# Kernel tuning notes

Hardware: AMD Instinct MI355X
Metric: run time of the kernel (lower is better)

The kernel has to match this reference:

```python
import jax, jax.numpy as jnp
import numpy as np

PATCH = 9  # patch_size (kernel_size=1, stride=1, padding=0, dilation_patch=1)


def setup_inputs() -> dict:
    key = jax.random.key(0)
    k1, k2 = jax.random.split(key)
    B, C, H, W = 4, 256, 128, 128
    return {
        "input1": jax.random.normal(k1, (B, C, H, W), dtype=jnp.float32),
        "input2": jax.random.normal(k2, (B, C, H, W), dtype=jnp.float32),
    }


def _correlation(input1, input2, patch=PATCH):
    # Faithful to torch _correlation_patch_based fast path:
    # corr[b, dy*P+dx, h, w] = sum_c input1[b,c,h,w] * input2_pad[b,c,h+dy,w+dx]
    # where input2 is zero-padded by P//2 (matches F.unfold padding=P//2).
    B, C, H, W = input1.shape
    pad = patch // 2
    i2p = jnp.pad(input2, ((0, 0), (0, 0), (pad, pad), (pad, pad)))
    # displacement offsets in unfold order: ky-major, kx-minor
    offs = jnp.stack(
        jnp.meshgrid(jnp.arange(patch), jnp.arange(patch), indexing="ij"), axis=-1
    ).reshape(-1, 2)  # (P*P, 2)

    def body(carry, off):
        # shifted window of input2, same (B,C,H,W) footprint (no unfold blowup)
        win = jax.lax.dynamic_slice(i2p, (0, 0, off[0], off[1]), (B, C, H, W))
        return carry, jnp.einsum("bchw,bchw->bhw", input1, win)

    _, corr = jax.lax.scan(body, None, offs)  # (P*P, B, H, W)
    return jnp.transpose(corr, (1, 0, 2, 3))  # (B, P*P, H, W)


def reference(input1, input2):
    return _correlation(input1, input2)
```

## Files before the change

### kernel.cpp

```cpp
#include <hip/hip_runtime.h>

#define BB   4
#define CC   256
#define HH   128
#define WW   128
#define PAD  4
#define KOUT 81

#define TH   8
#define SW   16
#define KC   32
#define NCHUNK (CC / KC)
#define AK   40

typedef _Float16 half8 __attribute__((ext_vector_type(8)));
typedef float    f32x4 __attribute__((ext_vector_type(4)));

__global__ __launch_bounds__(512, 4)
void corr_mfma4(const float* __restrict__ i1,
                const float* __restrict__ i2,
                float* __restrict__ out)
{
    __shared__ _Float16 Ald[128 * AK];
    __shared__ _Float16 Bld[512 * AK];

    const int t    = threadIdx.x;
    const int wave = t >> 6;
    const int lane = t & 63;
    const int l15  = lane & 15;
    const int quad = lane >> 4;

    const int raw     = blockIdx.x + 8 * blockIdx.y + 128 * blockIdx.z;
    const int logical = (raw & 7) * 64 + (raw >> 3);
    const int b  = logical >> 7;
    const int h0 = ((logical >> 3) & 15) * TH;
    const int w0 = (logical & 7) * SW;

    const size_t strideC = (size_t)HH * WW;
    const float* i1b = i1 + (size_t)b * CC * strideC;
    const float* i2b = i2 + (size_t)b * CC * strideC;

    bool valid;
    const float* gp;
    _Float16* ld0;

    if (t < 384) {
        const int g   = t % 6;
        const int t6  = t / 6;
        const int ch8 = t6 & 3;
        const int sr  = t6 >> 2;
        const int row  = h0 - PAD + sr;
        const int col0 = w0 - PAD + 4 * g;
        valid = (row >= 0) && (row < HH) && (col0 >= 0) && (col0 + 3 < WW);
        gp  = i2b + (size_t)(valid ? row : 0) * WW + (valid ? col0 : 0)
                  + (size_t)ch8 * 8 * strideC;
        ld0 = &Bld[(sr * 32 + 4 * g) * AK + ch8 * 8];
    } else {
        const int i   = t - 384;
        const int g   = i & 3;
        const int t4  = i >> 2;
        const int ch8 = t4 & 3;
        const int sr  = t4 >> 2;
        valid = true;
        gp  = i1b + (size_t)(h0 + sr) * WW + (w0 + 4 * g)
                  + (size_t)ch8 * 8 * strideC;
        ld0 = &Ald[(sr * 16 + 4 * g) * AK + ch8 * 8];
    }

    f32x4 acc[9][2];
#pragma unroll
    for (int dy = 0; dy < 9; ++dy) {
        acc[dy][0] = (f32x4){0.f, 0.f, 0.f, 0.f};
        acc[dy][1] = (f32x4){0.f, 0.f, 0.f, 0.f};
    }

    f32x4 L[8];

    if (valid) {
#pragma unroll
        for (int j = 0; j < 8; ++j)
            L[j] = *(const f32x4*)(gp + (size_t)j * strideC);
#pragma unroll
        for (int i = 0; i < 4; ++i) {
            half8 hv;
#pragma unroll
            for (int k = 0; k < 8; ++k) hv[k] = (_Float16)L[k][i];
            *(half8*)(ld0 + i * AK) = hv;
        }
    } else {
        const half8 z = (half8){0, 0, 0, 0, 0, 0, 0, 0};
#pragma unroll
        for (int i = 0; i < 4; ++i)
            *(half8*)(ld0 + i * AK) = z;
    }
    __syncthreads();

#pragma unroll 1
    for (int ch = 0; ch < NCHUNK; ++ch) {
        if (valid && (ch + 1 < NCHUNK)) {
            const float* gnext = gp + (size_t)(ch + 1) * KC * strideC;
#pragma unroll
            for (int j = 0; j < 8; ++j)
                L[j] = *(const f32x4*)(gnext + (size_t)j * strideC);
        }

        {
            const half8 a = *(const half8*)&Ald[(wave * 16 + l15) * AK + quad * 8];
#pragma unroll
            for (int dy = 0; dy < 9; ++dy) {
                const int r = wave + dy;
                const half8 b0 = *(const half8*)&Bld[(r * 32 + l15) * AK + quad * 8];
                acc[dy][0] = __builtin_amdgcn_mfma_f32_16x16x32_f16(a, b0, acc[dy][0], 0, 0, 0);
                const half8 b1 = *(const half8*)&Bld[(r * 32 + 16 + l15) * AK + quad * 8];
                acc[dy][1] = __builtin_amdgcn_mfma_f32_16x16x32_f16(a, b1, acc[dy][1], 0, 0, 0);
            }
        }

        if (ch + 1 < NCHUNK) {
            __syncthreads();
            if (valid) {
#pragma unroll
                for (int i = 0; i < 4; ++i) {
                    half8 hv;
#pragma unroll
                    for (int k = 0; k < 8; ++k) hv[k] = (_Float16)L[k][i];
                    *(half8*)(ld0 + i * AK) = hv;
                }
            }
            __syncthreads();
        }
    }

    const int h = h0 + wave;
#pragma unroll
    for (int dy = 0; dy < 9; ++dy) {
#pragma unroll
        for (int tt = 0; tt < 2; ++tt) {
#pragma unroll
            for (int reg = 0; reg < 4; ++reg) {
                const int p  = quad * 4 + reg;
                const int dx = l15 + 16 * tt - p;
                if (dx >= 0 && dx <= 8) {
                    out[(((size_t)b * KOUT + (dy * 9 + dx)) * HH + h) * WW + (w0 + p)] =
                        acc[dy][tt][reg];
                }
            }
        }
    }
}

extern "C" void kernel_launch(void* const* d_in, const int* in_sizes, int n_in,
                              void* d_out, int out_size, void* d_ws, size_t ws_size,
                              hipStream_t stream)
{
    (void)in_sizes; (void)n_in; (void)d_ws; (void)ws_size; (void)out_size;
    const float* i1 = (const float*)d_in[0];
    const float* i2 = (const float*)d_in[1];
    float* out = (float*)d_out;

    dim3 grid(WW / SW, HH / TH, BB);
    dim3 block(512);
    corr_mfma4<<<grid, block, 0, stream>>>(i1, i2, out);
}
```

Measured before the change: 178.1 us.

## Stage output through shared memory and interleave fp16 conversion between MFMA groups

```diff
diff --git a/kernel.cpp b/kernel.cpp
--- a/kernel.cpp
+++ b/kernel.cpp
@@ -12,17 +12,20 @@
 #define KC   32
 #define NCHUNK (CC / KC)
 #define AK   40
+#define SCP  130
 
 typedef _Float16 half8 __attribute__((ext_vector_type(8)));
 typedef float    f32x4 __attribute__((ext_vector_type(4)));
 
 __global__ __launch_bounds__(512, 4)
-void corr_mfma4(const float* __restrict__ i1,
+void corr_mfma5(const float* __restrict__ i1,
                 const float* __restrict__ i2,
                 float* __restrict__ out)
 {
-    __shared__ _Float16 Ald[128 * AK];
-    __shared__ _Float16 Bld[512 * AK];
+    __shared__ __align__(16) char smem[51200];
+    _Float16* const Ald = (_Float16*)smem;
+    _Float16* const Bld = (_Float16*)(smem + 10240);
+    float*    const sc  = (float*)smem;
 
     const int t    = threadIdx.x;
     const int wave = t >> 6;
@@ -74,18 +77,17 @@
         acc[dy][1] = (f32x4){0.f, 0.f, 0.f, 0.f};
     }
 
-    f32x4 L[8];
-
     if (valid) {
+        f32x4 L[8];
 #pragma unroll
         for (int j = 0; j < 8; ++j)
             L[j] = *(const f32x4*)(gp + (size_t)j * strideC);
 #pragma unroll
         for (int i = 0; i < 4; ++i) {
-            half8 hv;
+            half8 hvp;
 #pragma unroll
-            for (int k = 0; k < 8; ++k) hv[k] = (_Float16)L[k][i];
-            *(half8*)(ld0 + i * AK) = hv;
+            for (int k = 0; k < 8; ++k) hvp[k] = (_Float16)L[k][i];
+            *(half8*)(ld0 + i * AK) = hvp;
         }
     } else {
         const half8 z = (half8){0, 0, 0, 0, 0, 0, 0, 0};
@@ -95,43 +97,65 @@
     }
     __syncthreads();
 
+    half8 hv[4];
+
 #pragma unroll 1
     for (int ch = 0; ch < NCHUNK; ++ch) {
-        if (valid && (ch + 1 < NCHUNK)) {
-            const float* gnext = gp + (size_t)(ch + 1) * KC * strideC;
+        const bool more = (ch + 1 < NCHUNK);
+
+        f32x4 L[8];
+        if (valid && more) {
+            const float* g = gp + (size_t)(ch + 1) * KC * strideC;
 #pragma unroll
             for (int j = 0; j < 8; ++j)
-                L[j] = *(const f32x4*)(gnext + (size_t)j * strideC);
+                L[j] = *(const f32x4*)(g + (size_t)j * strideC);
         }
 
-        {
-            const half8 a = *(const half8*)&Ald[(wave * 16 + l15) * AK + quad * 8];
+        const half8 a = *(const half8*)&Ald[(wave * 16 + l15) * AK + quad * 8];
+
 #pragma unroll
-            for (int dy = 0; dy < 9; ++dy) {
-                const int r = wave + dy;
-                const half8 b0 = *(const half8*)&Bld[(r * 32 + l15) * AK + quad * 8];
-                acc[dy][0] = __builtin_amdgcn_mfma_f32_16x16x32_f16(a, b0, acc[dy][0], 0, 0, 0);
-                const half8 b1 = *(const half8*)&Bld[(r * 32 + 16 + l15) * AK + quad * 8];
-                acc[dy][1] = __builtin_amdgcn_mfma_f32_16x16x32_f16(a, b1, acc[dy][1], 0, 0, 0);
+        for (int dy = 0; dy < 5; ++dy) {
+            const int r = wave + dy;
+            const half8 b0 = *(const half8*)&Bld[(r * 32 + l15) * AK + quad * 8];
+            acc[dy][0] = __builtin_amdgcn_mfma_f32_16x16x32_f16(a, b0, acc[dy][0], 0, 0, 0);
+            const half8 b1 = *(const half8*)&Bld[(r * 32 + 16 + l15) * AK + quad * 8];
+            acc[dy][1] = __builtin_amdgcn_mfma_f32_16x16x32_f16(a, b1, acc[dy][1], 0, 0, 0);
+        }
+
+        if (valid && more) {
+#pragma unroll
+            for (int i = 0; i < 4; ++i) {
+#pragma unroll
+                for (int k = 0; k < 4; ++k) hv[i][k] = (_Float16)L[k][i];
+            }
+#pragma unroll
+            for (int i = 0; i < 4; ++i) {
+#pragma unroll
+                for (int k = 4; k < 8; ++k) hv[i][k] = (_Float16)L[k][i];
             }
         }
 
-        if (ch + 1 < NCHUNK) {
+#pragma unroll
+        for (int dy = 5; dy < 9; ++dy) {
+            const int r = wave + dy;
+            const half8 b0 = *(const half8*)&Bld[(r * 32 + l15) * AK + quad * 8];
+            acc[dy][0] = __builtin_amdgcn_mfma_f32_16x16x32_f16(a, b0, acc[dy][0], 0, 0, 0);
+            const half8 b1 = *(const half8*)&Bld[(r * 32 + 16 + l15) * AK + quad * 8];
+            acc[dy][1] = __builtin_amdgcn_mfma_f32_16x16x32_f16(a, b1, acc[dy][1], 0, 0, 0);
+        }
+
+        if (more) {
             __syncthreads();
             if (valid) {
 #pragma unroll
-                for (int i = 0; i < 4; ++i) {
-                    half8 hv;
-#pragma unroll
-                    for (int k = 0; k < 8; ++k) hv[k] = (_Float16)L[k][i];
-                    *(half8*)(ld0 + i * AK) = hv;
-                }
+                for (int i = 0; i < 4; ++i)
+                    *(half8*)(ld0 + i * AK) = hv[i];
             }
             __syncthreads();
         }
     }
 
-    const int h = h0 + wave;
+    __syncthreads();
 #pragma unroll
     for (int dy = 0; dy < 9; ++dy) {
 #pragma unroll
@@ -140,12 +164,19 @@
             for (int reg = 0; reg < 4; ++reg) {
                 const int p  = quad * 4 + reg;
                 const int dx = l15 + 16 * tt - p;
-                if (dx >= 0 && dx <= 8) {
-                    out[(((size_t)b * KOUT + (dy * 9 + dx)) * HH + h) * WW + (w0 + p)] =
-                        acc[dy][tt][reg];
-                }
+                if (dx >= 0 && dx <= 8)
+                    sc[(dy * 9 + dx) * SCP + wave * 16 + p] = acc[dy][tt][reg];
             }
         }
+    }
+    __syncthreads();
+
+    for (int k = wave; k < KOUT; k += TH) {
+        const float v0 = sc[k * SCP + lane];
+        const float v1 = sc[k * SCP + 64 + lane];
+        float* op = out + (((size_t)b * KOUT + k) * HH + h0) * WW + w0;
+        op[(size_t)(lane >> 4) * WW + (lane & 15)] = v0;
+        op[(size_t)(4 + (lane >> 4)) * WW + (lane & 15)] = v1;
     }
 }
 
@@ -160,5 +191,5 @@
 
     dim3 grid(WW / SW, HH / TH, BB);
     dim3 block(512);
-    corr_mfma4<<<grid, block, 0, stream>>>(i1, i2, out);
+    corr_mfma5<<<grid, block, 0, stream>>>(i1, i2, out);
 }
```

New measurement: 211.2 us. 18.6% more time.

## Halve row tile and split dy range across wave pairs

Applied to the files above, without the earlier changes.

```diff
diff --git a/kernel.cpp b/kernel.cpp
--- a/kernel.cpp
+++ b/kernel.cpp
@@ -7,44 +7,48 @@
 #define PAD  4
 #define KOUT 81
 
-#define TH   8
+#define TH   4
 #define SW   16
 #define KC   32
 #define NCHUNK (CC / KC)
 #define AK   40
+#define BROWS (TH + 8)
 
 typedef _Float16 half8 __attribute__((ext_vector_type(8)));
 typedef float    f32x4 __attribute__((ext_vector_type(4)));
 
 __global__ __launch_bounds__(512, 4)
-void corr_mfma4(const float* __restrict__ i1,
+void corr_mfma6(const float* __restrict__ i1,
                 const float* __restrict__ i2,
                 float* __restrict__ out)
 {
-    __shared__ _Float16 Ald[128 * AK];
-    __shared__ _Float16 Bld[512 * AK];
+    __shared__ __align__(16) _Float16 Ald[64 * AK];
+    __shared__ __align__(16) _Float16 Bld[384 * AK];
 
     const int t    = threadIdx.x;
     const int wave = t >> 6;
     const int lane = t & 63;
     const int l15  = lane & 15;
     const int quad = lane >> 4;
-
-    const int raw     = blockIdx.x + 8 * blockIdx.y + 128 * blockIdx.z;
-    const int logical = (raw & 7) * 64 + (raw >> 3);
-    const int b  = logical >> 7;
-    const int h0 = ((logical >> 3) & 15) * TH;
+    const int wr   = wave >> 1;
+    const int wd   = wave & 1;
+
+    const int raw     = blockIdx.x + 8 * blockIdx.y + 256 * blockIdx.z;
+    const int logical = (raw & 7) * 128 + (raw >> 3);
+    const int b  = logical >> 8;
+    const int h0 = ((logical >> 3) & 31) * TH;
     const int w0 = (logical & 7) * SW;
 
     const size_t strideC = (size_t)HH * WW;
     const float* i1b = i1 + (size_t)b * CC * strideC;
     const float* i2b = i2 + (size_t)b * CC * strideC;
 
-    bool valid;
+    bool stager, valid;
     const float* gp;
     _Float16* ld0;
 
-    if (t < 384) {
+    if (t < 288) {
+        stager = true;
         const int g   = t % 6;
         const int t6  = t / 6;
         const int ch8 = t6 & 3;
@@ -55,8 +59,9 @@
         gp  = i2b + (size_t)(valid ? row : 0) * WW + (valid ? col0 : 0)
                   + (size_t)ch8 * 8 * strideC;
         ld0 = &Bld[(sr * 32 + 4 * g) * AK + ch8 * 8];
-    } else {
-        const int i   = t - 384;
+    } else if (t < 352) {
+        stager = true;
+        const int i   = t - 288;
         const int g   = i & 3;
         const int t4  = i >> 2;
         const int ch8 = t4 & 3;
@@ -65,13 +70,18 @@
         gp  = i1b + (size_t)(h0 + sr) * WW + (w0 + 4 * g)
                   + (size_t)ch8 * 8 * strideC;
         ld0 = &Ald[(sr * 16 + 4 * g) * AK + ch8 * 8];
-    }
-
-    f32x4 acc[9][2];
-#pragma unroll
-    for (int dy = 0; dy < 9; ++dy) {
-        acc[dy][0] = (f32x4){0.f, 0.f, 0.f, 0.f};
-        acc[dy][1] = (f32x4){0.f, 0.f, 0.f, 0.f};
+    } else {
+        stager = false;
+        valid  = false;
+        gp  = i1b;
+        ld0 = &Ald[0];
+    }
+
+    f32x4 acc[5][2];
+#pragma unroll
+    for (int j = 0; j < 5; ++j) {
+        acc[j][0] = (f32x4){0.f, 0.f, 0.f, 0.f};
+        acc[j][1] = (f32x4){0.f, 0.f, 0.f, 0.f};
     }
 
     f32x4 L[8];
@@ -87,7 +97,7 @@
             for (int k = 0; k < 8; ++k) hv[k] = (_Float16)L[k][i];
             *(half8*)(ld0 + i * AK) = hv;
         }
-    } else {
+    } else if (stager) {
         const half8 z = (half8){0, 0, 0, 0, 0, 0, 0, 0};
 #pragma unroll
         for (int i = 0; i < 4; ++i)
@@ -97,26 +107,39 @@
 
 #pragma unroll 1
     for (int ch = 0; ch < NCHUNK; ++ch) {
-        if (valid && (ch + 1 < NCHUNK)) {
-            const float* gnext = gp + (size_t)(ch + 1) * KC * strideC;
+        const bool more = (ch + 1 < NCHUNK);
+
+        if (valid && more) {
+            const float* g = gp + (size_t)(ch + 1) * KC * strideC;
 #pragma unroll
             for (int j = 0; j < 8; ++j)
-                L[j] = *(const f32x4*)(gnext + (size_t)j * strideC);
+                L[j] = *(const f32x4*)(g + (size_t)j * strideC);
         }
 
         {
-            const half8 a = *(const half8*)&Ald[(wave * 16 + l15) * AK + quad * 8];
-#pragma unroll
-            for (int dy = 0; dy < 9; ++dy) {
-                const int r = wave + dy;
-                const half8 b0 = *(const half8*)&Bld[(r * 32 + l15) * AK + quad * 8];
-                acc[dy][0] = __builtin_amdgcn_mfma_f32_16x16x32_f16(a, b0, acc[dy][0], 0, 0, 0);
-                const half8 b1 = *(const half8*)&Bld[(r * 32 + 16 + l15) * AK + quad * 8];
-                acc[dy][1] = __builtin_amdgcn_mfma_f32_16x16x32_f16(a, b1, acc[dy][1], 0, 0, 0);
-            }
-        }
-
-        if (ch + 1 < NCHUNK) {
+            const half8 a = *(const half8*)&Ald[(wr * 16 + l15) * AK + quad * 8];
+            if (wd == 0) {
+#pragma unroll
+                for (int j = 0; j < 5; ++j) {
+                    const int r = wr + j;
+                    const half8 b0 = *(const half8*)&Bld[(r * 32 + l15) * AK + quad * 8];
+                    acc[j][0] = __builtin_amdgcn_mfma_f32_16x16x32_f16(a, b0, acc[j][0], 0, 0, 0);
+                    const half8 b1 = *(const half8*)&Bld[(r * 32 + 16 + l15) * AK + quad * 8];
+                    acc[j][1] = __builtin_amdgcn_mfma_f32_16x16x32_f16(a, b1, acc[j][1], 0, 0, 0);
+                }
+            } else {
+#pragma unroll
+                for (int j = 0; j < 4; ++j) {
+                    const int r = wr + 5 + j;
+                    const half8 b0 = *(const half8*)&Bld[(r * 32 + l15) * AK + quad * 8];
+                    acc[j][0] = __builtin_amdgcn_mfma_f32_16x16x32_f16(a, b0, acc[j][0], 0, 0, 0);
+                    const half8 b1 = *(const half8*)&Bld[(r * 32 + 16 + l15) * AK + quad * 8];
+                    acc[j][1] = __builtin_amdgcn_mfma_f32_16x16x32_f16(a, b1, acc[j][1], 0, 0, 0);
+                }
+            }
+        }
+
+        if (more) {
             __syncthreads();
             if (valid) {
 #pragma unroll
@@ -131,18 +154,38 @@
         }
     }
 
-    const int h = h0 + wave;
-#pragma unroll
-    for (int dy = 0; dy < 9; ++dy) {
-#pragma unroll
-        for (int tt = 0; tt < 2; ++tt) {
-#pragma unroll
-            for (int reg = 0; reg < 4; ++reg) {
-                const int p  = quad * 4 + reg;
-                const int dx = l15 + 16 * tt - p;
-                if (dx >= 0 && dx <= 8) {
-                    out[(((size_t)b * KOUT + (dy * 9 + dx)) * HH + h) * WW + (w0 + p)] =
-                        acc[dy][tt][reg];
+    const int h = h0 + wr;
+    if (wd == 0) {
+#pragma unroll
+        for (int j = 0; j < 5; ++j) {
+            const int dy = j;
+#pragma unroll
+            for (int tt = 0; tt < 2; ++tt) {
+#pragma unroll
+                for (int reg = 0; reg < 4; ++reg) {
+                    const int p  = quad * 4 + reg;
+                    const int dx = l15 + 16 * tt - p;
+                    if (dx >= 0 && dx <= 8) {
+                        out[(((size_t)b * KOUT + (dy * 9 + dx)) * HH + h) * WW + (w0 + p)] =
+                            acc[j][tt][reg];
+                    }
+                }
+            }
+        }
+    } else {
+#pragma unroll
+        for (int j = 0; j < 4; ++j) {
+            const int dy = 5 + j;
+#pragma unroll
+            for (int tt = 0; tt < 2; ++tt) {
+#pragma unroll
+                for (int reg = 0; reg < 4; ++reg) {
+                    const int p  = quad * 4 + reg;
+                    const int dx = l15 + 16 * tt - p;
+                    if (dx >= 0 && dx <= 8) {
+                        out[(((size_t)b * KOUT + (dy * 9 + dx)) * HH + h) * WW + (w0 + p)] =
+                            acc[j][tt][reg];
+                    }
                 }
             }
         }
@@ -160,5 +203,5 @@
 
     dim3 grid(WW / SW, HH / TH, BB);
     dim3 block(512);
-    corr_mfma4<<<grid, block, 0, stream>>>(i1, i2, out);
+    corr_mfma6<<<grid, block, 0, stream>>>(i1, i2, out);
 }
```

Result: slower. 190.0 us (+6.7%).
